# Optimization experiments

Measured on AMD Instinct MI355X. Metric: run time of the kernel, lower is better.

## Reference

```python
import jax, jax.numpy as jnp
import numpy as np

CLASS_NUM = 80
NUM_PRED = 2
TOPK = 1000
LEVEL_SIZES = [147456, 36864, 9216, 2304, 576]


def _make_anchors(key, n):
    k1, k2, k3, k4 = jax.random.split(key, 4)
    x1 = jax.random.uniform(k1, (n,)) * 1000.0
    y1 = jax.random.uniform(k2, (n,)) * 1000.0
    w = jax.random.uniform(k3, (n,)) * 200.0 + 8.0
    h = jax.random.uniform(k4, (n,)) * 200.0 + 8.0
    return jnp.stack([x1, y1, x1 + w, y1 + h], axis=1)


def setup_inputs() -> dict:
    key = jax.random.key(0)
    inp = {}
    for i, n in enumerate(LEVEL_SIZES):
        ka = jax.random.fold_in(key, 3 * i)
        kc = jax.random.fold_in(key, 3 * i + 1)
        kr = jax.random.fold_in(key, 3 * i + 2)
        inp[f"anchors{i}"] = _make_anchors(ka, n)
        inp[f"cls{i}"] = jax.random.normal(kc, (1, n, CLASS_NUM * NUM_PRED), dtype=jnp.float32)
        inp[f"reg{i}"] = jax.random.normal(kr, (1, n, 4 * NUM_PRED), dtype=jnp.float32) * 0.1
    return inp


def bbox_transform_inv(anchors, deltas):
    # anchors: [N,4] (x1,y1,x2,y2); deltas: [N,4] (dx,dy,dw,dh)
    w = anchors[:, 2] - anchors[:, 0] + 1.0
    h = anchors[:, 3] - anchors[:, 1] + 1.0
    cx = anchors[:, 0] + 0.5 * w
    cy = anchors[:, 1] + 0.5 * h
    pcx = cx + deltas[:, 0] * w
    pcy = cy + deltas[:, 1] * h
    pw = w * jnp.exp(deltas[:, 2])
    ph = h * jnp.exp(deltas[:, 3])
    return jnp.stack([pcx - 0.5 * pw, pcy - 0.5 * ph,
                      pcx + 0.5 * pw, pcy + 0.5 * ph], axis=1)


def _per_layer_inference(anchors_list, cls_list, reg_list):
    keep_a, keep_c, keep_r = [], [], []
    for a, c, r in zip(anchors_list, cls_list, reg_list):
        a = a.reshape(-1, 4)
        c = c[0].reshape(-1, CLASS_NUM * NUM_PRED)
        r = r[0].reshape(-1, 4 * NUM_PRED)
        if a.shape[0] > TOPK:
            ruler = jnp.max(c, axis=1)
            _, inds = jax.lax.top_k(ruler, TOPK)
            a, c, r = a[inds], c[inds], r[inds]
        keep_a.append(a)
        keep_c.append(jax.nn.sigmoid(c))
        keep_r.append(r)
    a = jnp.concatenate(keep_a, axis=0)   # [N,4]
    c = jnp.concatenate(keep_c, axis=0)   # [N, C*P]
    r = jnp.concatenate(keep_r, axis=0)   # [N, 4*P]
    n = a.shape[0]
    tag = (jnp.arange(CLASS_NUM, dtype=a.dtype) + 1.0)
    tag = jnp.tile(tag[None, :], (n, 1)).reshape(-1, 1)  # [N*C,1]
    scores0 = c[:, :CLASS_NUM].reshape(-1, 1)
    scores1 = c[:, CLASS_NUM:].reshape(-1, 1)
    bbox0 = bbox_transform_inv(a, r[:, :4])
    bbox1 = bbox_transform_inv(a, r[:, 4:])
    bbox0 = jnp.tile(bbox0, (1, CLASS_NUM)).reshape(-1, 4)
    bbox1 = jnp.tile(bbox1, (1, CLASS_NUM)).reshape(-1, 4)
    pred0 = jnp.concatenate([bbox0, scores0, tag], axis=1)
    pred1 = jnp.concatenate([bbox1, scores1, tag], axis=1)
    return jnp.concatenate([pred0, pred1], axis=1)  # [N*C, 12]


def reference(anchors0, anchors1, anchors2, anchors3, anchors4,
              cls0, cls1, cls2, cls3, cls4,
              reg0, reg1, reg2, reg3, reg4):
    return _per_layer_inference(
        [anchors0, anchors1, anchors2, anchors3, anchors4],
        [cls0, cls1, cls2, cls3, cls4],
        [reg0, reg1, reg2, reg3, reg4])
```

## Files before the change

kernel.cpp:

```cpp
#include <hip/hip_runtime.h>

#define CLS   160
#define TOPKN 1000
#define N0 147456
#define N1 36864
#define N2 9216
#define N3 2304
#define N4 576
#define NROWS (N0 + N1 + N2 + N3)
#define BD1 N0
#define BD2 (N0 + N1)
#define BD3 (N0 + N1 + N2)
#define NSEL (4 * TOPKN + N4)
#define NBINS 65536
#define CAND_CAP 2048

__device__ __forceinline__ unsigned sortable(float f) {
    unsigned u = __float_as_uint(f);
    return (u & 0x80000000u) ? ~u : (u | 0x80000000u);
}

__global__ __launch_bounds__(256) void k_ruler(
    const float* __restrict__ c0, const float* __restrict__ c1,
    const float* __restrict__ c2, const float* __restrict__ c3,
    unsigned* __restrict__ keys, unsigned* __restrict__ hist)
{
    int tid  = blockIdx.x * 256 + threadIdx.x;
    if (tid < 4 * NBINS) hist[tid] = 0;

    int wv   = tid >> 6;
    int lane = tid & 63;
    int sub  = lane >> 3;
    int col  = lane & 7;
    const int NW = 1530 * 4;
    for (int g = wv; g < NROWS / 8; g += NW) {
        int r0 = g * 8;
        const float* cb; int lr;
        if (r0 < BD1)      { cb = c0; lr = r0; }
        else if (r0 < BD2) { cb = c1; lr = r0 - BD1; }
        else if (r0 < BD3) { cb = c2; lr = r0 - BD2; }
        else               { cb = c3; lr = r0 - BD3; }
        const float4* p = (const float4*)cb + (size_t)(lr + sub) * 40 + col;
        float m = -3.4e38f;
        #pragma unroll
        for (int k = 0; k < 5; ++k) {
            float4 v = p[8 * k];
            m = fmaxf(m, fmaxf(fmaxf(v.x, v.y), fmaxf(v.z, v.w)));
        }
        m = fmaxf(m, __shfl_xor(m, 1));
        m = fmaxf(m, __shfl_xor(m, 2));
        m = fmaxf(m, __shfl_xor(m, 4));
        if (col == 0) keys[r0 + sub] = sortable(m);
    }
}

__global__ __launch_bounds__(256) void k_hist(const unsigned* __restrict__ keys,
                                              unsigned* __restrict__ hist)
{
    int b        = blockIdx.x;
    int level    = b >> 8;
    unsigned seg = (b >> 4) & 15;
    int chunk    = b & 15;
    __shared__ unsigned cnt[4096];
    for (int i = threadIdx.x; i < 4096; i += 256) cnt[i] = 0;
    __syncthreads();
    int base, n;
    switch (level) {
        case 0:  base = 0;   n = N0; break;
        case 1:  base = BD1; n = N1; break;
        case 2:  base = BD2; n = N2; break;
        default: base = BD3; n = N3; break;
    }
    int q = n >> 4;
    const uint4* kp = (const uint4*)(keys + base + chunk * q);
    int nv = q >> 2;
    for (int i = threadIdx.x; i < nv; i += 256) {
        uint4 k = kp[i];
        unsigned b0 = k.x >> 16, b1 = k.y >> 16, b2 = k.z >> 16, b3 = k.w >> 16;
        if ((b0 >> 12) == seg) atomicAdd(&cnt[b0 & 4095u], 1u);
        if ((b1 >> 12) == seg) atomicAdd(&cnt[b1 & 4095u], 1u);
        if ((b2 >> 12) == seg) atomicAdd(&cnt[b2 & 4095u], 1u);
        if ((b3 >> 12) == seg) atomicAdd(&cnt[b3 & 4095u], 1u);
    }
    __syncthreads();
    unsigned* h = hist + level * NBINS + (seg << 12);
    for (int i = threadIdx.x; i < 4096; i += 256) {
        unsigned c = cnt[i];
        if (c) atomicAdd(&h[i], c);
    }
}

__global__ __launch_bounds__(1024) void k_decide(const unsigned* __restrict__ hist,
                                                 unsigned* __restrict__ ctrl)
{
    int level = blockIdx.x;
    const unsigned* h = hist + level * NBINS;
    int t = threadIdx.x;
    __shared__ unsigned s[1024];

    unsigned sum = 0;
    #pragma unroll 4
    for (int i = 0; i < 64; ++i) sum += h[t * 64 + i];
    s[t] = sum;
    __syncthreads();

    for (int off = 1; off < 1024; off <<= 1) {
        unsigned v   = s[t];
        unsigned add = (t + off < 1024) ? s[t + off] : 0u;
        __syncthreads();
        s[t] = v + add;
        __syncthreads();
    }

    if (s[t] >= TOPKN && (t == 1023 || s[t + 1] < TOPKN)) {
        unsigned cum = (t == 1023) ? 0u : s[t + 1];
        int edge = t * 64;
        for (int b = t * 64 + 63; b >= t * 64; --b) {
            cum += h[b];
            if (cum >= TOPKN) { edge = b; break; }
        }
        ctrl[level]     = ((unsigned)edge) << 16;
        ctrl[4 + level] = 0u;
    }
}

__global__ __launch_bounds__(256) void k_compact(const unsigned* __restrict__ keys,
                                                 unsigned* __restrict__ ctrl,
                                                 uint2* __restrict__ cand)
{
    int w = blockIdx.x * 256 + threadIdx.x;
    int lane = threadIdx.x & 63;
    int level, base;
    if (w < BD1)      { level = 0; base = 0;   }
    else if (w < BD2) { level = 1; base = BD1; }
    else if (w < BD3) { level = 2; base = BD2; }
    else              { level = 3; base = BD3; }
    unsigned key = keys[w];
    bool pass = key >= ctrl[level];
    unsigned long long mask = __ballot(pass);
    if (pass) {
        int leader    = __ffsll((long long)mask) - 1;
        unsigned tot  = (unsigned)__popcll(mask);
        unsigned rank = (unsigned)__popcll(mask & ((1ull << lane) - 1ull));
        unsigned bpos = 0;
        if (lane == leader) bpos = atomicAdd(&ctrl[4 + level], tot);
        bpos = (unsigned)__shfl((int)bpos, leader);
        unsigned pos = bpos + rank;
        if (pos < CAND_CAP)
            cand[level * CAND_CAP + pos] = make_uint2(key, (unsigned)(w - base));
    }
}

__global__ __launch_bounds__(1024) void k_rank(const uint2* __restrict__ cand,
                                               const unsigned* __restrict__ ctrl,
                                               unsigned* __restrict__ sel)
{
    int level = blockIdx.x;
    unsigned cnt = ctrl[4 + level];
    if (cnt > CAND_CAP) cnt = CAND_CAP;
    __shared__ unsigned long long a[CAND_CAP];
    for (int i = threadIdx.x; i < (int)cnt; i += 1024) {
        uint2 c = cand[level * CAND_CAP + i];
        a[i] = ((unsigned long long)c.x << 32) | (unsigned)(~c.y);
    }
    __syncthreads();
    for (int i = threadIdx.x; i < (int)cnt; i += 1024) {
        unsigned long long mine = a[i];
        unsigned rank = 0;
        for (int j = 0; j < (int)cnt; ++j) rank += (a[j] > mine) ? 1u : 0u;
        if (rank < TOPKN)
            sel[level * TOPKN + rank] = ~(unsigned)(mine & 0xFFFFFFFFull);
    }
}

__global__ __launch_bounds__(256) void k_epilogue(
    const float* a0, const float* a1, const float* a2, const float* a3, const float* a4,
    const float* c0, const float* c1, const float* c2, const float* c3, const float* c4,
    const float* r0, const float* r1, const float* r2, const float* r3, const float* r4,
    const unsigned* __restrict__ sel, float* __restrict__ out)
{
    int s = blockIdx.x;
    int level, idx;
    if (s < 4 * TOPKN) {
        level = s / TOPKN;
        idx   = (int)sel[s];
    } else {
        level = 4;
        idx   = s - 4 * TOPKN;
    }
    const float *A, *C, *R;
    switch (level) {
        case 0: A = a0; C = c0; R = r0; break;
        case 1: A = a1; C = c1; R = r1; break;
        case 2: A = a2; C = c2; R = r2; break;
        case 3: A = a3; C = c3; R = r3; break;
        default: A = a4; C = c4; R = r4; break;
    }

    __shared__ float sc[CLS];
    __shared__ float bb[8];

    const float* cp = C + (size_t)idx * CLS;
    if (threadIdx.x < CLS) {
        float x = cp[threadIdx.x];
        sc[threadIdx.x] = 1.0f / (1.0f + __expf(-x));
    }
    if (threadIdx.x == 192) {
        const float* ap = A + (size_t)idx * 4;
        const float* rp = R + (size_t)idx * 8;
        float x1 = ap[0], y1 = ap[1], x2 = ap[2], y2 = ap[3];
        float w  = x2 - x1 + 1.0f, h = y2 - y1 + 1.0f;
        float cx = x1 + 0.5f * w,  cy = y1 + 0.5f * h;
        #pragma unroll
        for (int p = 0; p < 2; ++p) {
            float pcx = cx + rp[4 * p + 0] * w;
            float pcy = cy + rp[4 * p + 1] * h;
            float pw  = w * __expf(rp[4 * p + 2]);
            float ph  = h * __expf(rp[4 * p + 3]);
            bb[4 * p + 0] = pcx - 0.5f * pw;
            bb[4 * p + 1] = pcy - 0.5f * ph;
            bb[4 * p + 2] = pcx + 0.5f * pw;
            bb[4 * p + 3] = pcy + 0.5f * ph;
        }
    }
    __syncthreads();

    float4* orow = (float4*)(out + (size_t)s * 960);
    if (threadIdx.x < 240) {
        int j = threadIdx.x / 3, part = threadIdx.x % 3;
        float tag = (float)(j + 1);
        float4 v;
        if (part == 0)      v = make_float4(bb[0], bb[1], bb[2], bb[3]);
        else if (part == 1) v = make_float4(sc[j], tag, bb[4], bb[5]);
        else                v = make_float4(bb[6], bb[7], sc[80 + j], tag);
        orow[threadIdx.x] = v;
    }
}

extern "C" void kernel_launch(void* const* d_in, const int* in_sizes, int n_in,
                              void* d_out, int out_size, void* d_ws, size_t ws_size,
                              hipStream_t stream)
{
    bool interleaved = (in_sizes[1] > 1000000);
    const float *A[5], *C[5], *R[5];
    for (int i = 0; i < 5; ++i) {
        if (interleaved) {
            A[i] = (const float*)d_in[3 * i + 0];
            C[i] = (const float*)d_in[3 * i + 1];
            R[i] = (const float*)d_in[3 * i + 2];
        } else {
            A[i] = (const float*)d_in[i];
            C[i] = (const float*)d_in[5 + i];
            R[i] = (const float*)d_in[10 + i];
        }
    }

    unsigned* keys = (unsigned*)d_ws;
    unsigned* hist = keys + NROWS;
    unsigned* ctrl = hist + 4 * NBINS;
    uint2*    cand = (uint2*)(ctrl + 8);
    unsigned* sel  = (unsigned*)(cand + 4 * CAND_CAP);

    k_ruler<<<1530, 256, 0, stream>>>(C[0], C[1], C[2], C[3], keys, hist);
    k_hist<<<1024, 256, 0, stream>>>(keys, hist);
    k_decide<<<4, 1024, 0, stream>>>(hist, ctrl);
    k_compact<<<NROWS / 256, 256, 0, stream>>>(keys, ctrl, cand);
    k_rank<<<4, 1024, 0, stream>>>(cand, ctrl, sel);
    k_epilogue<<<NSEL, 256, 0, stream>>>(A[0], A[1], A[2], A[3], A[4],
                                         C[0], C[1], C[2], C[3], C[4],
                                         R[0], R[1], R[2], R[3], R[4],
                                         sel, (float*)d_out);
}
```

Before: 101.1 us.

## Fuse threshold decision, compaction and ranking into one per-level select kernel

```diff
diff --git a/kernel.cpp b/kernel.cpp
--- a/kernel.cpp
+++ b/kernel.cpp
@@ -25,22 +25,24 @@
     const float* __restrict__ c2, const float* __restrict__ c3,
     unsigned* __restrict__ keys, unsigned* __restrict__ hist)
 {
-    int tid  = blockIdx.x * 256 + threadIdx.x;
+    int tid = blockIdx.x * 256 + threadIdx.x;
     if (tid < 4 * NBINS) hist[tid] = 0;
 
-    int wv   = tid >> 6;
-    int lane = tid & 63;
+    int r0 = blockIdx.x << 7;
+    const float* cb; int lr0;
+    if (r0 < BD1)      { cb = c0; lr0 = r0; }
+    else if (r0 < BD2) { cb = c1; lr0 = r0 - BD1; }
+    else if (r0 < BD3) { cb = c2; lr0 = r0 - BD2; }
+    else               { cb = c3; lr0 = r0 - BD3; }
+
+    int wv   = threadIdx.x >> 6;
+    int lane = threadIdx.x & 63;
     int sub  = lane >> 3;
     int col  = lane & 7;
-    const int NW = 1530 * 4;
-    for (int g = wv; g < NROWS / 8; g += NW) {
-        int r0 = g * 8;
-        const float* cb; int lr;
-        if (r0 < BD1)      { cb = c0; lr = r0; }
-        else if (r0 < BD2) { cb = c1; lr = r0 - BD1; }
-        else if (r0 < BD3) { cb = c2; lr = r0 - BD2; }
-        else               { cb = c3; lr = r0 - BD3; }
-        const float4* p = (const float4*)cb + (size_t)(lr + sub) * 40 + col;
+    #pragma unroll
+    for (int i = 0; i < 4; ++i) {
+        int rrel = wv * 32 + i * 8 + sub;
+        const float4* p = (const float4*)cb + (size_t)(lr0 + rrel) * 40 + col;
         float m = -3.4e38f;
         #pragma unroll
         for (int k = 0; k < 5; ++k) {
@@ -50,7 +52,7 @@
         m = fmaxf(m, __shfl_xor(m, 1));
         m = fmaxf(m, __shfl_xor(m, 2));
         m = fmaxf(m, __shfl_xor(m, 4));
-        if (col == 0) keys[r0 + sub] = sortable(m);
+        if (col == 0) keys[r0 + rrel] = sortable(m);
     }
 }
 
@@ -90,20 +92,25 @@
     }
 }
 
-__global__ __launch_bounds__(1024) void k_decide(const unsigned* __restrict__ hist,
-                                                 unsigned* __restrict__ ctrl)
+__global__ __launch_bounds__(1024) void k_select(const unsigned* __restrict__ keys,
+                                                 const unsigned* __restrict__ hist,
+                                                 unsigned* __restrict__ sel)
 {
     int level = blockIdx.x;
+    int t     = threadIdx.x;
+    int lane  = t & 63;
     const unsigned* h = hist + level * NBINS;
-    int t = threadIdx.x;
+
     __shared__ unsigned s[1024];
+    __shared__ unsigned long long a[CAND_CAP];
+    __shared__ unsigned thr_s, cnt_s;
 
     unsigned sum = 0;
     #pragma unroll 4
     for (int i = 0; i < 64; ++i) sum += h[t * 64 + i];
     s[t] = sum;
-    __syncthreads();
-
+    if (t == 0) cnt_s = 0;
+    __syncthreads();
     for (int off = 1; off < 1024; off <<= 1) {
         unsigned v   = s[t];
         unsigned add = (t + off < 1024) ? s[t + off] : 0u;
@@ -111,7 +118,6 @@
         s[t] = v + add;
         __syncthreads();
     }
-
     if (s[t] >= TOPKN && (t == 1023 || s[t + 1] < TOPKN)) {
         unsigned cum = (t == 1023) ? 0u : s[t + 1];
         int edge = t * 64;
@@ -119,52 +125,46 @@
             cum += h[b];
             if (cum >= TOPKN) { edge = b; break; }
         }
-        ctrl[level]     = ((unsigned)edge) << 16;
-        ctrl[4 + level] = 0u;
-    }
-}
-
-__global__ __launch_bounds__(256) void k_compact(const unsigned* __restrict__ keys,
-                                                 unsigned* __restrict__ ctrl,
-                                                 uint2* __restrict__ cand)
-{
-    int w = blockIdx.x * 256 + threadIdx.x;
-    int lane = threadIdx.x & 63;
-    int level, base;
-    if (w < BD1)      { level = 0; base = 0;   }
-    else if (w < BD2) { level = 1; base = BD1; }
-    else if (w < BD3) { level = 2; base = BD2; }
-    else              { level = 3; base = BD3; }
-    unsigned key = keys[w];
-    bool pass = key >= ctrl[level];
-    unsigned long long mask = __ballot(pass);
-    if (pass) {
-        int leader    = __ffsll((long long)mask) - 1;
-        unsigned tot  = (unsigned)__popcll(mask);
-        unsigned rank = (unsigned)__popcll(mask & ((1ull << lane) - 1ull));
-        unsigned bpos = 0;
-        if (lane == leader) bpos = atomicAdd(&ctrl[4 + level], tot);
-        bpos = (unsigned)__shfl((int)bpos, leader);
-        unsigned pos = bpos + rank;
-        if (pos < CAND_CAP)
-            cand[level * CAND_CAP + pos] = make_uint2(key, (unsigned)(w - base));
-    }
-}
-
-__global__ __launch_bounds__(1024) void k_rank(const uint2* __restrict__ cand,
-                                               const unsigned* __restrict__ ctrl,
-                                               unsigned* __restrict__ sel)
-{
-    int level = blockIdx.x;
-    unsigned cnt = ctrl[4 + level];
+        thr_s = ((unsigned)edge) << 16;
+    }
+    __syncthreads();
+    unsigned thr = thr_s;
+
+    int base, n;
+    switch (level) {
+        case 0:  base = 0;   n = N0; break;
+        case 1:  base = BD1; n = N1; break;
+        case 2:  base = BD2; n = N2; break;
+        default: base = BD3; n = N3; break;
+    }
+    const uint4* kp = (const uint4*)(keys + base);
+    int nv = n >> 2;
+    for (int i = t; i < nv; i += 1024) {
+        uint4 k4 = kp[i];
+        unsigned kv[4] = {k4.x, k4.y, k4.z, k4.w};
+        #pragma unroll
+        for (int c = 0; c < 4; ++c) {
+            bool pass = kv[c] >= thr;
+            unsigned long long mask = __ballot(pass);
+            if (pass) {
+                int leader    = __ffsll((long long)mask) - 1;
+                unsigned tot  = (unsigned)__popcll(mask);
+                unsigned rank = (unsigned)__popcll(mask & ((1ull << lane) - 1ull));
+                unsigned bp = 0;
+                if (lane == leader) bp = atomicAdd(&cnt_s, tot);
+                bp = (unsigned)__shfl((int)bp, leader);
+                unsigned pos = bp + rank;
+                if (pos < CAND_CAP)
+                    a[pos] = ((unsigned long long)kv[c] << 32) |
+                             (unsigned)~(unsigned)(4 * i + c);
+            }
+        }
+    }
+    __syncthreads();
+    unsigned cnt = cnt_s;
     if (cnt > CAND_CAP) cnt = CAND_CAP;
-    __shared__ unsigned long long a[CAND_CAP];
-    for (int i = threadIdx.x; i < (int)cnt; i += 1024) {
-        uint2 c = cand[level * CAND_CAP + i];
-        a[i] = ((unsigned long long)c.x << 32) | (unsigned)(~c.y);
-    }
-    __syncthreads();
-    for (int i = threadIdx.x; i < (int)cnt; i += 1024) {
+
+    for (int i = t; i < (int)cnt; i += 1024) {
         unsigned long long mine = a[i];
         unsigned rank = 0;
         for (int j = 0; j < (int)cnt; ++j) rank += (a[j] > mine) ? 1u : 0u;
@@ -257,15 +257,11 @@
 
     unsigned* keys = (unsigned*)d_ws;
     unsigned* hist = keys + NROWS;
-    unsigned* ctrl = hist + 4 * NBINS;
-    uint2*    cand = (uint2*)(ctrl + 8);
-    unsigned* sel  = (unsigned*)(cand + 4 * CAND_CAP);
+    unsigned* sel  = hist + 4 * NBINS;
 
     k_ruler<<<1530, 256, 0, stream>>>(C[0], C[1], C[2], C[3], keys, hist);
     k_hist<<<1024, 256, 0, stream>>>(keys, hist);
-    k_decide<<<4, 1024, 0, stream>>>(hist, ctrl);
-    k_compact<<<NROWS / 256, 256, 0, stream>>>(keys, ctrl, cand);
-    k_rank<<<4, 1024, 0, stream>>>(cand, ctrl, sel);
+    k_select<<<4, 1024, 0, stream>>>(keys, hist, sel);
     k_epilogue<<<NSEL, 256, 0, stream>>>(A[0], A[1], A[2], A[3], A[4],
                                          C[0], C[1], C[2], C[3], C[4],
                                          R[0], R[1], R[2], R[3], R[4],
```

After: 89.45 us. 1.13x faster.
